# Optimization experiments

Measured on AMD Instinct MI355X. Metric: run time of the kernel, lower is better.

## Reference

```python
import jax, jax.numpy as jnp
import numpy as np

EPS = 1e-06


def elu_plus_one(x):
    # F.elu(x) + 1 == exp(x) for x < 0, x + 1 for x >= 0 (alpha=1)
    return jnp.where(x > 0, x + 1.0, jnp.exp(jnp.minimum(x, 0.0)))


def safe_divide(a, b, eps=EPS):
    return a / (b + eps)


def setup_inputs() -> dict:
    key0 = jax.random.key(0)
    kq, kk, kv, kM, kz = jax.random.split(key0, 5)
    B, H, S, D = 4, 16, 4096, 128
    query = jax.random.normal(kq, (B, H, S, D), dtype=jnp.float32)
    key = jax.random.normal(kk, (B, H, S, D), dtype=jnp.float32)
    value = jax.random.normal(kv, (B, H, S, D), dtype=jnp.float32)
    M = jax.random.normal(kM, (B, H, D, D), dtype=jnp.float32)
    z = jax.random.uniform(kz, (B, H, D, 1), dtype=jnp.float32)
    return {"query": query, "key": key, "value": value, "M": M, "z": z}


def reference(query, key, value, M, z):
    # --- update (delta rule) ---
    sigma_k = elu_plus_one(key)                       # [B,H,S,D]
    mem_pred = jnp.einsum('bhsd,bhde->bhse', sigma_k, M)   # sigma(K) @ M
    normalizer = jnp.einsum('bhsd,bhdo->bhso', sigma_k, z) # sigma(K) @ z -> [B,H,S,1]
    delta_v = value - safe_divide(mem_pred, normalizer)
    M_new = M + jnp.einsum('bhsd,bhse->bhde', sigma_k, delta_v)  # sigma(K)^T @ delta_V
    z_new = z + jnp.sum(sigma_k, axis=2)[..., None]              # [B,H,D,1]

    # --- retrieve with updated memory ---
    sigma_q = elu_plus_one(query)
    mem_out = jnp.einsum('bhsd,bhde->bhse', sigma_q, M_new)
    norm_q = jnp.einsum('bhsd,bhdo->bhso', sigma_q, z_new)
    out = safe_divide(mem_out, norm_q)                # [B,H,S,D]
    return out, M_new, z_new
```

## Files before the change

kernel.cpp:

```cpp
#include <hip/hip_runtime.h>
#include <math.h>

#define D 128
#define EPS 1e-6f
#define SKR_LD 136
#define SKT_LD 40
#define DV_LD  40
#define SKR_SZ (32 * SKR_LD)
#define SKT_SZ (128 * SKT_LD)

typedef __attribute__((ext_vector_type(8))) short short8;
typedef __attribute__((ext_vector_type(4))) float f32x4;
typedef unsigned short ushort_t;
typedef unsigned long long u64;

__device__ __forceinline__ float elu1(float x) {
    float e = __expf(fminf(x, 0.f));
    return x > 0.f ? x + 1.f : e;
}
__device__ __forceinline__ unsigned short bf16rne(float f) {
    unsigned u = __builtin_bit_cast(unsigned, f);
    u += 0x7FFFu + ((u >> 16) & 1u);
    return (unsigned short)(u >> 16);
}
__device__ __forceinline__ u64 pack4(float a, float b, float c, float d) {
    return (u64)bf16rne(a) | ((u64)bf16rne(b) << 16) |
           ((u64)bf16rne(c) << 32) | ((u64)bf16rne(d) << 48);
}

__global__ __launch_bounds__(512, 4)
void k_update(const float* __restrict__ key, const float* __restrict__ value,
              const float* __restrict__ M, const float* __restrict__ z,
              float* __restrict__ pM, float* __restrict__ pz, int S)
{
    __shared__ alignas(16) ushort_t skR[2 * SKR_SZ];
    __shared__ alignas(16) ushort_t skT[2 * SKT_SZ];
    __shared__ alignas(16) ushort_t dvT[128 * DV_LD];

    const int t  = threadIdx.x;
    const int bh = blockIdx.x, ch = blockIdx.y, NCH = gridDim.y;
    const int SC = S / NCH, NB = SC / 32, s0g = ch * SC;

    const int w = t >> 6, g = (t >> 4) & 3, m = t & 15;
    const int c2 = t & 63;

    const float* Kb = key   + (size_t)bh * S * D;
    const float* Vb = value + (size_t)bh * S * D;
    const float* Mb = M + (size_t)bh * D * D;
    const float* zb = z + (size_t)bh * D;

    short8 Bf[4], zf[4];
    #pragma unroll
    for (int ks = 0; ks < 4; ++ks) {
        short8 f, zfr;
        #pragma unroll
        for (int j = 0; j < 8; ++j) {
            f[j]   = (short)bf16rne(Mb[(size_t)(32 * ks + 8 * g + j) * D + 16 * w + m]);
            zfr[j] = (short)bf16rne(zb[32 * ks + 8 * g + j]);
        }
        Bf[ks] = f; zf[ks] = zfr;
    }

    f32x4 acc[8];
    #pragma unroll
    for (int dt = 0; dt < 8; ++dt) acc[dt] = 0.f;
    float zacc0 = 0.f, zacc1 = 0.f;

    auto STAGE = [&](const float2* kr, int buf) {
        float sv0[4], sv1[4];
        #pragma unroll
        for (int i = 0; i < 4; ++i) { sv0[i] = elu1(kr[i].x); sv1[i] = elu1(kr[i].y); }
        #pragma unroll
        for (int i = 0; i < 4; ++i)
            *(unsigned*)&skR[buf * SKR_SZ + (4 * w + i) * SKR_LD + 2 * c2] =
                (unsigned)bf16rne(sv0[i]) | ((unsigned)bf16rne(sv1[i]) << 16);
        *(u64*)&skT[buf * SKT_SZ + (2 * c2) * SKT_LD + 4 * w] =
            pack4(sv0[0], sv0[1], sv0[2], sv0[3]);
        *(u64*)&skT[buf * SKT_SZ + (2 * c2 + 1) * SKT_LD + 4 * w] =
            pack4(sv1[0], sv1[1], sv1[2], sv1[3]);
        zacc0 += sv0[0] + sv0[1] + sv0[2] + sv0[3];
        zacc1 += sv1[0] + sv1[1] + sv1[2] + sv1[3];
    };

    {
        float2 kr[4];
        #pragma unroll
        for (int i = 0; i < 4; ++i)
            kr[i] = *(const float2*)&Kb[(size_t)(s0g + 4 * w + i) * D + 2 * c2];
        STAGE(kr, 0);
    }
    __syncthreads();

    for (int b = 0; b < NB; ++b) {
        const int cur = b & 1;
        const int sbat = s0g + 32 * b;

        float2 kr[4];
        if (b + 1 < NB) {
            #pragma unroll
            for (int i = 0; i < 4; ++i)
                kr[i] = *(const float2*)&Kb[(size_t)(sbat + 32 + 4 * w + i) * D + 2 * c2];
        }

        float vv[2][4];
        #pragma unroll
        for (int st = 0; st < 2; ++st)
            #pragma unroll
            for (int r = 0; r < 4; ++r)
                vv[st][r] = Vb[(size_t)(sbat + 16 * st + 4 * g + r) * D + 16 * w + m];

        f32x4 mp[2], mz[2];
        #pragma unroll
        for (int st = 0; st < 2; ++st) { mp[st] = 0.f; mz[st] = 0.f; }
        #pragma unroll
        for (int st = 0; st < 2; ++st)
            #pragma unroll
            for (int ks = 0; ks < 4; ++ks) {
                short8 a = *(short8*)&skR[cur * SKR_SZ + (16 * st + m) * SKR_LD + 32 * ks + 8 * g];
                mp[st] = __builtin_amdgcn_mfma_f32_16x16x32_bf16(a, Bf[ks], mp[st], 0, 0, 0);
                mz[st] = __builtin_amdgcn_mfma_f32_16x16x32_bf16(a, zf[ks], mz[st], 0, 0, 0);
            }

        #pragma unroll
        for (int st = 0; st < 2; ++st) {
            float dv[4];
            #pragma unroll
            for (int r = 0; r < 4; ++r)
                dv[r] = vv[st][r] - mp[st][r] / (mz[st][r] + EPS);
            *(u64*)&dvT[(16 * w + m) * DV_LD + 16 * st + 4 * g] =
                pack4(dv[0], dv[1], dv[2], dv[3]);
        }
        asm volatile("" ::: "memory");

        short8 bfr = *(short8*)&dvT[(16 * w + m) * DV_LD + 8 * g];

        #pragma unroll
        for (int dt = 0; dt < 8; ++dt) {
            short8 a2 = *(short8*)&skT[cur * SKT_SZ + (16 * dt + m) * SKT_LD + 8 * g];
            acc[dt] = __builtin_amdgcn_mfma_f32_16x16x32_bf16(a2, bfr, acc[dt], 0, 0, 0);
        }

        if (b + 1 < NB) STAGE(kr, cur ^ 1);
        __syncthreads();
    }

    float* pMb = pM + ((size_t)bh * NCH + ch) * (D * D);
    #pragma unroll
    for (int dt = 0; dt < 8; ++dt)
        #pragma unroll
        for (int r = 0; r < 4; ++r)
            pMb[(size_t)(16 * dt + 4 * g + r) * D + 16 * w + m] = acc[dt][r];

    float* zsc = (float*)skR;
    zsc[w * 128 + 2 * c2]     = zacc0;
    zsc[w * 128 + 2 * c2 + 1] = zacc1;
    __syncthreads();
    if (t < 128) {
        float a = 0.f;
        #pragma unroll
        for (int r = 0; r < 8; ++r) a += zsc[r * 128 + t];
        pz[((size_t)bh * NCH + ch) * D + t] = a;
    }
}

__global__ void k_reduce(const float* __restrict__ M, const float* __restrict__ z,
                         const float* __restrict__ pM, const float* __restrict__ pz,
                         float* __restrict__ Mnew, float* __restrict__ znew, int NCH)
{
    const int bh = blockIdx.x, sl = blockIdx.y, t = threadIdx.x;
    const size_t baseM = (size_t)bh * D * D;
    for (int i = sl * 2048 + t; i < (sl + 1) * 2048; i += 256) {
        float a = M[baseM + i];
        for (int c = 0; c < NCH; ++c) a += pM[((size_t)bh * NCH + c) * (D * D) + i];
        Mnew[baseM + i] = a;
    }
    if (sl == 0 && t < D) {
        float a = z[(size_t)bh * D + t];
        for (int c = 0; c < NCH; ++c) a += pz[((size_t)bh * NCH + c) * D + t];
        znew[(size_t)bh * D + t] = a;
    }
}

__global__ __launch_bounds__(256, 2)
void k_retrieve(const float* __restrict__ query, const float* __restrict__ Mnew,
                const float* __restrict__ znew, float* __restrict__ out, int S)
{
    __shared__ alignas(16) ushort_t sqR[2][32 * SKR_LD];
    __shared__ float normsh[2][32];

    const int t  = threadIdx.x;
    const int bh = blockIdx.x, ch = blockIdx.y, NCH = gridDim.y;
    const int SC = S / NCH;
    const int NB = SC / 32;
    const int s0g = ch * SC;

    const int w = t >> 6, g = (t >> 4) & 3, m = t & 15;
    const int sb = t >> 5, db = t & 31;

    const float* Qb = query + (size_t)bh * S * D;
    const float* Mb = Mnew + (size_t)bh * D * D;
    const float* zb = znew + (size_t)bh * D;
    float*       Ob = out + (size_t)bh * S * D;

    float zr[4];
    #pragma unroll
    for (int j = 0; j < 4; ++j) zr[j] = zb[4 * db + j];

    short8 Bf[4][2];
    #pragma unroll
    for (int ks = 0; ks < 4; ++ks)
        #pragma unroll
        for (int p = 0; p < 2; ++p) {
            short8 f;
            #pragma unroll
            for (int j = 0; j < 8; ++j)
                f[j] = (short)bf16rne(Mb[(size_t)(32 * ks + 8 * g + j) * D + 16 * (2 * w + p) + m]);
            Bf[ks][p] = f;
        }

    auto STAGE_PROC = [&](const float4* qreg, int bu) {
        float sv[4][4];
        #pragma unroll
        for (int js = 0; js < 4; ++js) {
            sv[js][0] = elu1(qreg[js].x); sv[js][1] = elu1(qreg[js].y);
            sv[js][2] = elu1(qreg[js].z); sv[js][3] = elu1(qreg[js].w);
        }
        #pragma unroll
        for (int js = 0; js < 4; ++js)
            *(u64*)&sqR[bu][(4 * sb + js) * SKR_LD + 4 * db] =
                pack4(sv[js][0], sv[js][1], sv[js][2], sv[js][3]);
        float np[4];
        #pragma unroll
        for (int js = 0; js < 4; ++js)
            np[js] = sv[js][0] * zr[0] + sv[js][1] * zr[1] +
                     sv[js][2] * zr[2] + sv[js][3] * zr[3];
        #pragma unroll
        for (int mask = 16; mask >= 1; mask >>= 1) {
            np[0] += __shfl_xor(np[0], mask, 64);
            np[1] += __shfl_xor(np[1], mask, 64);
            np[2] += __shfl_xor(np[2], mask, 64);
            np[3] += __shfl_xor(np[3], mask, 64);
        }
        if (db < 4) {
            float v = db == 0 ? np[0] : db == 1 ? np[1] : db == 2 ? np[2] : np[3];
            normsh[bu][4 * sb + db] = v + EPS;
        }
    };

    {
        float4 qreg[4];
        #pragma unroll
        for (int js = 0; js < 4; ++js)
            qreg[js] = *(const float4*)&Qb[(size_t)(s0g + 4 * sb + js) * D + 4 * db];
        STAGE_PROC(qreg, 0);
    }
    __syncthreads();

    for (int b = 0; b < NB; ++b) {
        const int bu = b & 1;
        float4 qreg[4];
        if (b + 1 < NB) {
            #pragma unroll
            for (int js = 0; js < 4; ++js)
                qreg[js] = *(const float4*)&Qb[(size_t)(s0g + 32 * (b + 1) + 4 * sb + js) * D + 4 * db];
        }

        f32x4 mp[2][2];
        #pragma unroll
        for (int st = 0; st < 2; ++st)
            #pragma unroll
            for (int p = 0; p < 2; ++p) mp[st][p] = 0.f;
        #pragma unroll
        for (int st = 0; st < 2; ++st)
            #pragma unroll
            for (int ks = 0; ks < 4; ++ks) {
                short8 a = *(short8*)&sqR[bu][(16 * st + m) * SKR_LD + 32 * ks + 8 * g];
                #pragma unroll
                for (int p = 0; p < 2; ++p)
                    mp[st][p] = __builtin_amdgcn_mfma_f32_16x16x32_bf16(a, Bf[ks][p], mp[st][p], 0, 0, 0);
            }

        #pragma unroll
        for (int st = 0; st < 2; ++st)
            #pragma unroll
            for (int r = 0; r < 4; ++r) {
                float rn = 1.f / normsh[bu][16 * st + 4 * g + r];
                #pragma unroll
                for (int p = 0; p < 2; ++p)
                    Ob[(size_t)(s0g + 32 * b + 16 * st + 4 * g + r) * D + 16 * (2 * w + p) + m] =
                        mp[st][p][r] * rn;
            }

        if (b + 1 < NB) STAGE_PROC(qreg, (b + 1) & 1);
        __syncthreads();
    }
}

extern "C" void kernel_launch(void* const* d_in, const int* in_sizes, int n_in,
                              void* d_out, int out_size, void* d_ws, size_t ws_size,
                              hipStream_t stream)
{
    const float* q = (const float*)d_in[0];
    const float* k = (const float*)d_in[1];
    const float* v = (const float*)d_in[2];
    const float* M = (const float*)d_in[3];
    const float* z = (const float*)d_in[4];

    const int BH = in_sizes[3] / (D * D);
    const int S  = in_sizes[0] / (BH * D);

    float* out  = (float*)d_out;
    float* Mnew = out + (size_t)BH * S * D;
    float* znew = Mnew + (size_t)BH * D * D;

    int NCH = 8;
    const size_t per_set = (size_t)BH * (D * D + D) * sizeof(float);
    while (NCH > 1 && (size_t)NCH * per_set > ws_size) NCH >>= 1;

    float* pM;
    float* pz;
    if ((size_t)NCH * per_set <= ws_size) {
        pM = (float*)d_ws;
        pz = pM + (size_t)NCH * BH * D * D;
    } else {
        NCH = 1;
        pM = Mnew;
        pz = znew;
    }

    dim3 gridA(BH, NCH);
    k_update<<<gridA, 512, 0, stream>>>(k, v, M, z, pM, pz, S);
    dim3 gridB(BH, 8);
    k_reduce<<<gridB, 256, 0, stream>>>(M, z, pM, pz, Mnew, znew, NCH);
    dim3 gridC(BH, 8);
    k_retrieve<<<gridC, 256, 0, stream>>>(q, Mnew, znew, out, S);
}
```

Before: 157.4 us.

## Single-buffer LDS staging, compute normalizer via shuffles, prefetch V, raise chunk count

The update kernel drops the double-buffered LDS staging of sigma(K) and uses a single buffer with an extra barrier per iteration. This shrinks LDS so six blocks can fit per CU instead of four. The normalizer sigma(K)·z is now computed in fp32 with wave shuffles into shared memory, replacing the extra MFMA against a bf16 z fragment. Value loads are prefetched one batch ahead, and the sequence is split into 16 chunks instead of 8 for more parallelism, at the cost of more partial-sum reduction traffic.

```diff
diff --git a/kernel.cpp b/kernel.cpp
--- a/kernel.cpp
+++ b/kernel.cpp
@@ -28,14 +28,15 @@
            ((u64)bf16rne(c) << 32) | ((u64)bf16rne(d) << 48);
 }
 
-__global__ __launch_bounds__(512, 4)
+__global__ __launch_bounds__(512, 6)
 void k_update(const float* __restrict__ key, const float* __restrict__ value,
               const float* __restrict__ M, const float* __restrict__ z,
               float* __restrict__ pM, float* __restrict__ pz, int S)
 {
-    __shared__ alignas(16) ushort_t skR[2 * SKR_SZ];
-    __shared__ alignas(16) ushort_t skT[2 * SKT_SZ];
+    __shared__ alignas(16) ushort_t skR[SKR_SZ];
+    __shared__ alignas(16) ushort_t skT[SKT_SZ];
     __shared__ alignas(16) ushort_t dvT[128 * DV_LD];
+    __shared__ float normsh[32];
 
     const int t  = threadIdx.x;
     const int bh = blockIdx.x, ch = blockIdx.y, NCH = gridDim.y;
@@ -49,16 +50,16 @@
     const float* Mb = M + (size_t)bh * D * D;
     const float* zb = z + (size_t)bh * D;
 
-    short8 Bf[4], zf[4];
+    const float zr0 = zb[2 * c2], zr1 = zb[2 * c2 + 1];
+
+    short8 Bf[4];
     #pragma unroll
     for (int ks = 0; ks < 4; ++ks) {
-        short8 f, zfr;
-        #pragma unroll
-        for (int j = 0; j < 8; ++j) {
-            f[j]   = (short)bf16rne(Mb[(size_t)(32 * ks + 8 * g + j) * D + 16 * w + m]);
-            zfr[j] = (short)bf16rne(zb[32 * ks + 8 * g + j]);
-        }
-        Bf[ks] = f; zf[ks] = zfr;
+        short8 f;
+        #pragma unroll
+        for (int j = 0; j < 8; ++j)
+            f[j] = (short)bf16rne(Mb[(size_t)(32 * ks + 8 * g + j) * D + 16 * w + m]);
+        Bf[ks] = f;
     }
 
     f32x4 acc[8];
@@ -66,59 +67,79 @@
     for (int dt = 0; dt < 8; ++dt) acc[dt] = 0.f;
     float zacc0 = 0.f, zacc1 = 0.f;
 
-    auto STAGE = [&](const float2* kr, int buf) {
+    auto STAGE = [&](const float2* kr) {
         float sv0[4], sv1[4];
         #pragma unroll
         for (int i = 0; i < 4; ++i) { sv0[i] = elu1(kr[i].x); sv1[i] = elu1(kr[i].y); }
         #pragma unroll
         for (int i = 0; i < 4; ++i)
-            *(unsigned*)&skR[buf * SKR_SZ + (4 * w + i) * SKR_LD + 2 * c2] =
+            *(unsigned*)&skR[(4 * w + i) * SKR_LD + 2 * c2] =
                 (unsigned)bf16rne(sv0[i]) | ((unsigned)bf16rne(sv1[i]) << 16);
-        *(u64*)&skT[buf * SKT_SZ + (2 * c2) * SKT_LD + 4 * w] =
-            pack4(sv0[0], sv0[1], sv0[2], sv0[3]);
-        *(u64*)&skT[buf * SKT_SZ + (2 * c2 + 1) * SKT_LD + 4 * w] =
-            pack4(sv1[0], sv1[1], sv1[2], sv1[3]);
-        zacc0 += sv0[0] + sv0[1] + sv0[2] + sv0[3];
-        zacc1 += sv1[0] + sv1[1] + sv1[2] + sv1[3];
+        *(u64*)&skT[(2 * c2) * SKT_LD + 4 * w]     = pack4(sv0[0], sv0[1], sv0[2], sv0[3]);
+        *(u64*)&skT[(2 * c2 + 1) * SKT_LD + 4 * w] = pack4(sv1[0], sv1[1], sv1[2], sv1[3]);
+        float p[4];
+        #pragma unroll
+        for (int i = 0; i < 4; ++i) {
+            p[i] = sv0[i] * zr0 + sv1[i] * zr1;
+            zacc0 += sv0[i]; zacc1 += sv1[i];
+        }
+        #pragma unroll
+        for (int mask = 32; mask >= 1; mask >>= 1) {
+            p[0] += __shfl_xor(p[0], mask, 64);
+            p[1] += __shfl_xor(p[1], mask, 64);
+            p[2] += __shfl_xor(p[2], mask, 64);
+            p[3] += __shfl_xor(p[3], mask, 64);
+        }
+        int l = t & 63;
+        if (l < 4) {
+            float pv = l == 0 ? p[0] : l == 1 ? p[1] : l == 2 ? p[2] : p[3];
+            normsh[4 * w + l] = pv + EPS;
+        }
     };
 
-    {
-        float2 kr[4];
+    float2 kr[4];
+    #pragma unroll
+    for (int i = 0; i < 4; ++i)
+        kr[i] = *(const float2*)&Kb[(size_t)(s0g + 4 * w + i) * D + 2 * c2];
+    STAGE(kr);
+    if (NB > 1) {
         #pragma unroll
         for (int i = 0; i < 4; ++i)
-            kr[i] = *(const float2*)&Kb[(size_t)(s0g + 4 * w + i) * D + 2 * c2];
-        STAGE(kr, 0);
-    }
+            kr[i] = *(const float2*)&Kb[(size_t)(s0g + 32 + 4 * w + i) * D + 2 * c2];
+    }
+    float vn[2][4];
+    #pragma unroll
+    for (int st = 0; st < 2; ++st)
+        #pragma unroll
+        for (int r = 0; r < 4; ++r)
+            vn[st][r] = Vb[(size_t)(s0g + 16 * st + 4 * g + r) * D + 16 * w + m];
     __syncthreads();
 
     for (int b = 0; b < NB; ++b) {
-        const int cur = b & 1;
         const int sbat = s0g + 32 * b;
 
-        float2 kr[4];
+        float vv[2][4];
+        #pragma unroll
+        for (int st = 0; st < 2; ++st)
+            #pragma unroll
+            for (int r = 0; r < 4; ++r) vv[st][r] = vn[st][r];
+
         if (b + 1 < NB) {
             #pragma unroll
-            for (int i = 0; i < 4; ++i)
-                kr[i] = *(const float2*)&Kb[(size_t)(sbat + 32 + 4 * w + i) * D + 2 * c2];
-        }
-
-        float vv[2][4];
-        #pragma unroll
-        for (int st = 0; st < 2; ++st)
-            #pragma unroll
-            for (int r = 0; r < 4; ++r)
-                vv[st][r] = Vb[(size_t)(sbat + 16 * st + 4 * g + r) * D + 16 * w + m];
-
-        f32x4 mp[2], mz[2];
-        #pragma unroll
-        for (int st = 0; st < 2; ++st) { mp[st] = 0.f; mz[st] = 0.f; }
+            for (int st = 0; st < 2; ++st)
+                #pragma unroll
+                for (int r = 0; r < 4; ++r)
+                    vn[st][r] = Vb[(size_t)(sbat + 32 + 16 * st + 4 * g + r) * D + 16 * w + m];
+        }
+
+        f32x4 mp[2];
+        mp[0] = 0.f; mp[1] = 0.f;
         #pragma unroll
         for (int st = 0; st < 2; ++st)
             #pragma unroll
             for (int ks = 0; ks < 4; ++ks) {
-                short8 a = *(short8*)&skR[cur * SKR_SZ + (16 * st + m) * SKR_LD + 32 * ks + 8 * g];
+                short8 a = *(short8*)&skR[(16 * st + m) * SKR_LD + 32 * ks + 8 * g];
                 mp[st] = __builtin_amdgcn_mfma_f32_16x16x32_bf16(a, Bf[ks], mp[st], 0, 0, 0);
-                mz[st] = __builtin_amdgcn_mfma_f32_16x16x32_bf16(a, zf[ks], mz[st], 0, 0, 0);
             }
 
         #pragma unroll
@@ -126,7 +147,7 @@
             float dv[4];
             #pragma unroll
             for (int r = 0; r < 4; ++r)
-                dv[r] = vv[st][r] - mp[st][r] / (mz[st][r] + EPS);
+                dv[r] = vv[st][r] - mp[st][r] / normsh[16 * st + 4 * g + r];
             *(u64*)&dvT[(16 * w + m) * DV_LD + 16 * st + 4 * g] =
                 pack4(dv[0], dv[1], dv[2], dv[3]);
         }
@@ -136,11 +157,20 @@
 
         #pragma unroll
         for (int dt = 0; dt < 8; ++dt) {
-            short8 a2 = *(short8*)&skT[cur * SKT_SZ + (16 * dt + m) * SKT_LD + 8 * g];
+            short8 a2 = *(short8*)&skT[(16 * dt + m) * SKT_LD + 8 * g];
             acc[dt] = __builtin_amdgcn_mfma_f32_16x16x32_bf16(a2, bfr, acc[dt], 0, 0, 0);
         }
 
-        if (b + 1 < NB) STAGE(kr, cur ^ 1);
+        __syncthreads();
+
+        if (b + 1 < NB) {
+            STAGE(kr);
+            if (b + 2 < NB) {
+                #pragma unroll
+                for (int i = 0; i < 4; ++i)
+                    kr[i] = *(const float2*)&Kb[(size_t)(sbat + 64 + 4 * w + i) * D + 2 * c2];
+            }
+        }
         __syncthreads();
     }
 
@@ -313,7 +343,7 @@
     float* Mnew = out + (size_t)BH * S * D;
     float* znew = Mnew + (size_t)BH * D * D;
 
-    int NCH = 8;
+    int NCH = 16;
     const size_t per_set = (size_t)BH * (D * D + D) * sizeof(float);
     while (NCH > 1 && (size_t)NCH * per_set > ws_size) NCH >>= 1;
 
```

After: 461.3 us. 2.93x slower.

## Prefetch K and V one batch ahead, use lighter barrier, double chunk count

Applied to the files above, without the earlier changes.

Software-pipelines the update kernel so that the next batch's K and V global loads are issued a full iteration ahead, keeping them in registers across the MFMA work. The __syncthreads is replaced with an inline s_waitcnt lgkmcnt(0)+s_barrier so the barrier does not wait on outstanding global loads, and an extra sync is added before the zsc scratch reuse. NCH is raised from 8 to 16 to put more blocks on the update pass. The trade-off is higher register pressure, and more partial sums for the reduce kernel to combine.

```diff
diff --git a/kernel.cpp b/kernel.cpp
--- a/kernel.cpp
+++ b/kernel.cpp
@@ -74,40 +74,46 @@
         for (int i = 0; i < 4; ++i)
             *(unsigned*)&skR[buf * SKR_SZ + (4 * w + i) * SKR_LD + 2 * c2] =
                 (unsigned)bf16rne(sv0[i]) | ((unsigned)bf16rne(sv1[i]) << 16);
-        *(u64*)&skT[buf * SKT_SZ + (2 * c2) * SKT_LD + 4 * w] =
-            pack4(sv0[0], sv0[1], sv0[2], sv0[3]);
-        *(u64*)&skT[buf * SKT_SZ + (2 * c2 + 1) * SKT_LD + 4 * w] =
-            pack4(sv1[0], sv1[1], sv1[2], sv1[3]);
+        *(u64*)&skT[buf * SKT_SZ + (2 * c2) * SKT_LD + 4 * w]     = pack4(sv0[0], sv0[1], sv0[2], sv0[3]);
+        *(u64*)&skT[buf * SKT_SZ + (2 * c2 + 1) * SKT_LD + 4 * w] = pack4(sv1[0], sv1[1], sv1[2], sv1[3]);
         zacc0 += sv0[0] + sv0[1] + sv0[2] + sv0[3];
         zacc1 += sv1[0] + sv1[1] + sv1[2] + sv1[3];
     };
 
-    {
-        float2 kr[4];
+    float2 kr[4];
+    #pragma unroll
+    for (int i = 0; i < 4; ++i)
+        kr[i] = *(const float2*)&Kb[(size_t)(s0g + 4 * w + i) * D + 2 * c2];
+    STAGE(kr, 0);
+    if (NB > 1) {
         #pragma unroll
         for (int i = 0; i < 4; ++i)
-            kr[i] = *(const float2*)&Kb[(size_t)(s0g + 4 * w + i) * D + 2 * c2];
-        STAGE(kr, 0);
-    }
+            kr[i] = *(const float2*)&Kb[(size_t)(s0g + 32 + 4 * w + i) * D + 2 * c2];
+    }
+    float vn[2][4];
+    #pragma unroll
+    for (int st = 0; st < 2; ++st)
+        #pragma unroll
+        for (int r = 0; r < 4; ++r)
+            vn[st][r] = Vb[(size_t)(s0g + 16 * st + 4 * g + r) * D + 16 * w + m];
     __syncthreads();
 
     for (int b = 0; b < NB; ++b) {
         const int cur = b & 1;
         const int sbat = s0g + 32 * b;
 
-        float2 kr[4];
+        float vv[2][4];
+        #pragma unroll
+        for (int st = 0; st < 2; ++st)
+            #pragma unroll
+            for (int r = 0; r < 4; ++r) vv[st][r] = vn[st][r];
         if (b + 1 < NB) {
             #pragma unroll
-            for (int i = 0; i < 4; ++i)
-                kr[i] = *(const float2*)&Kb[(size_t)(sbat + 32 + 4 * w + i) * D + 2 * c2];
-        }
-
-        float vv[2][4];
-        #pragma unroll
-        for (int st = 0; st < 2; ++st)
-            #pragma unroll
-            for (int r = 0; r < 4; ++r)
-                vv[st][r] = Vb[(size_t)(sbat + 16 * st + 4 * g + r) * D + 16 * w + m];
+            for (int st = 0; st < 2; ++st)
+                #pragma unroll
+                for (int r = 0; r < 4; ++r)
+                    vn[st][r] = Vb[(size_t)(sbat + 32 + 16 * st + 4 * g + r) * D + 16 * w + m];
+        }
 
         f32x4 mp[2], mz[2];
         #pragma unroll
@@ -140,8 +146,16 @@
             acc[dt] = __builtin_amdgcn_mfma_f32_16x16x32_bf16(a2, bfr, acc[dt], 0, 0, 0);
         }
 
-        if (b + 1 < NB) STAGE(kr, cur ^ 1);
-        __syncthreads();
+        if (b + 1 < NB) {
+            STAGE(kr, cur ^ 1);
+            if (b + 2 < NB) {
+                #pragma unroll
+                for (int i = 0; i < 4; ++i)
+                    kr[i] = *(const float2*)&Kb[(size_t)(sbat + 64 + 4 * w + i) * D + 2 * c2];
+            }
+        }
+
+        asm volatile("s_waitcnt lgkmcnt(0)\n\ts_barrier" ::: "memory");
     }
 
     float* pMb = pM + ((size_t)bh * NCH + ch) * (D * D);
@@ -151,6 +165,7 @@
         for (int r = 0; r < 4; ++r)
             pMb[(size_t)(16 * dt + 4 * g + r) * D + 16 * w + m] = acc[dt][r];
 
+    __syncthreads();
     float* zsc = (float*)skR;
     zsc[w * 128 + 2 * c2]     = zacc0;
     zsc[w * 128 + 2 * c2 + 1] = zacc1;
@@ -313,7 +328,7 @@
     float* Mnew = out + (size_t)BH * S * D;
     float* znew = Mnew + (size_t)BH * D * D;
 
-    int NCH = 8;
+    int NCH = 16;
     const size_t per_set = (size_t)BH * (D * D + D) * sizeof(float);
     while (NCH > 1 && (size_t)NCH * per_set > ws_size) NCH >>= 1;
 
```

After: 179.8 us. 1.14x slower.
